# Kernel optimization log

Measured on AMD Instinct MI355X. Metric: run time of the kernel, lower is better.

## Reference

```python
import jax, jax.numpy as jnp
import numpy as np

# Dimensions (see shape_source)
B, N, F = 2, 400, 246          # batch, nodes, node features
S = 1                           # edge feature channels
C = 32                          # stack_channels
LBL = 1440                      # shape_node_labels
STACK_IN = 2 * F + 2 * S        # concat([x_i, x_j, e_ij, e_ji])
NODE_IN = F + 2 * C             # concat([x, agg_in, agg_out])


def _glorot(key, shape):
    fan_in, fan_out = shape[0], shape[1]
    lim = np.sqrt(6.0 / (fan_in + fan_out)).astype(np.float32)
    return jax.random.uniform(key, shape, jnp.float32, -lim, lim)


def setup_inputs() -> dict:
    key = jax.random.key(0)
    ks = jax.random.split(key, 12)
    x = jax.random.normal(ks[0], (B, N, F), jnp.float32)
    a = (jax.random.uniform(ks[1], (B, N, N)) < 0.10).astype(jnp.float32)
    e = jax.random.uniform(ks[2], (B, N, N, S), jnp.float32)
    return {
        "x": x,
        "a": a,
        "e": e,
        # XENetConv stack model: single Dense(C) + PReLU (per-channel alpha)
        "W_stack": _glorot(ks[3], (STACK_IN, C)),
        "b_stack": jnp.zeros((C,), jnp.float32),
        "alpha": jnp.full((C,), 0.25, jnp.float32),
        # attention heads: Dense(1, sigmoid) each
        "W_att_i": _glorot(ks[4], (C, 1)),
        "b_att_i": jnp.zeros((1,), jnp.float32),
        "W_att_j": _glorot(ks[5], (C, 1)),
        "b_att_j": jnp.zeros((1,), jnp.float32),
        # node model: Dense(F) over concat([x, agg_in, agg_out]) (linear)
        "W_node": _glorot(ks[6], (NODE_IN, F)),
        "b_node": jnp.zeros((F,), jnp.float32),
        # trailing Dense(shape_node_labels, linear)
        "W_out": _glorot(ks[7], (F, LBL)),
        "b_out": jnp.zeros((LBL,), jnp.float32),
    }


def reference(x, a, e, W_stack, b_stack, alpha, W_att_i, b_att_i,
              W_att_j, b_att_j, W_node, b_node, W_out, b_out):
    # --- XENetConvBatch ---
    # pairwise stack: [x_i, x_j, e_ij, e_ji] over all (i, j) node pairs
    x_i = jnp.broadcast_to(x[:, :, None, :], (B, N, N, F))
    x_j = jnp.broadcast_to(x[:, None, :, :], (B, N, N, F))
    e_t = jnp.transpose(e, (0, 2, 1, 3))                     # e_ji
    stack = jnp.concatenate([x_i, x_j, e, e_t], axis=-1)     # (B,N,N,2F+2S)
    s = jnp.einsum("bijk,kc->bijc", stack, W_stack) + b_stack  # (B,N,N,C)
    s = jnp.where(s >= 0, s, alpha * s)                      # PReLU
    s = s * a[..., None]                                     # mask non-edges
    # attention (sigmoid gates for incoming / outgoing aggregation)
    att_i = jax.nn.sigmoid(s @ W_att_i + b_att_i)            # (B,N,N,1)
    att_j = jax.nn.sigmoid(s @ W_att_j + b_att_j)
    agg_i = jnp.sum(s * att_i, axis=2)                       # (B,N,C) sum over j
    agg_j = jnp.sum(s * att_j, axis=1)                       # (B,N,C) sum over i
    x_new = jnp.concatenate([x, agg_i, agg_j], axis=-1) @ W_node + b_node  # (B,N,F)
    # Net discards the edge output of the conv; final linear Dense
    out = x_new @ W_out + b_out                              # (B,N,LBL)
    return out
```

## Files before the change

### kernel.cpp

```cpp
#include <hip/hip_runtime.h>
#include <math.h>

#define B_ 2
#define N_ 400
#define F_ 246
#define C_ 32
#define LBL_ 1440

#define KX_ 320
#define KN_ 256

typedef __attribute__((ext_vector_type(8))) short bf16x8;
typedef __attribute__((ext_vector_type(4))) float f32x4;

__device__ __forceinline__ short f2bf(float f) {
    unsigned u = __float_as_uint(f);
    return (short)((u + 0x7FFF + ((u >> 16) & 1)) >> 16);
}

#define T_ABUF (800 * KX_)
#define T_W2T  (64 * KX_)
#define T_WNT  (256 * KX_)
#define T_WOT  (LBL_ * KN_)
__global__ void k_prep(const float* __restrict__ x, const float* __restrict__ Ws,
                       const float* __restrict__ Wn, const float* __restrict__ Wo,
                       short* __restrict__ Abuf, short* __restrict__ W2T,
                       short* __restrict__ WnT, short* __restrict__ WoT) {
    int t = blockIdx.x * 256 + threadIdx.x;
    if (t < T_ABUF) {
        int row = t / KX_, k = t % KX_;
        Abuf[t] = (k < F_) ? f2bf(x[row * F_ + k]) : (short)0;
        return;
    }
    t -= T_ABUF;
    if (t < T_W2T) {
        int n = t / KX_, k = t % KX_;
        float v = 0.f;
        if (k < F_) v = (n < C_) ? Ws[k * C_ + n] : Ws[(F_ + k) * C_ + (n - C_)];
        W2T[t] = f2bf(v);
        return;
    }
    t -= T_W2T;
    if (t < T_WNT) {
        int n = t / KX_, k = t % KX_;
        float v = (n < F_ && k < F_ + 2 * C_) ? Wn[k * F_ + n] : 0.f;
        WnT[t] = f2bf(v);
        return;
    }
    t -= T_WNT;
    if (t < T_WOT) {
        int n = t / KN_, k = t % KN_;
        WoT[t] = (k < F_) ? f2bf(Wo[k * LBL_ + n]) : (short)0;
    }
}

template <int K>
__device__ __forceinline__ f32x4 mfma_tile(const short* __restrict__ A,
                                           const short* __restrict__ BT,
                                           int m0, int n0, int lane) {
    int r = lane & 15, quad = lane >> 4;
    const short* ap = A + (size_t)(m0 + r) * K + quad * 8;
    const short* bp = BT + (size_t)(n0 + r) * K + quad * 8;
    f32x4 acc = {0.f, 0.f, 0.f, 0.f};
    #pragma unroll
    for (int kk = 0; kk < K; kk += 32) {
        bf16x8 a = *(const bf16x8*)(ap + kk);
        bf16x8 b = *(const bf16x8*)(bp + kk);
        acc = __builtin_amdgcn_mfma_f32_16x16x32_bf16(a, b, acc, 0, 0, 0);
    }
    return acc;
}

__global__ void k_pq(const short* __restrict__ Abuf, const short* __restrict__ W2T,
                     float* __restrict__ PQ) {
    int lane = threadIdx.x;
    int m0 = blockIdx.x * 16, n0 = blockIdx.y * 16;
    f32x4 acc = mfma_tile<KX_>(Abuf, W2T, m0, n0, lane);
    int n = n0 + (lane & 15), mb = m0 + (lane >> 4) * 4;
    #pragma unroll
    for (int reg = 0; reg < 4; ++reg)
        PQ[(size_t)(mb + reg) * 64 + n] = acc[reg];
}

__global__ void k_agg(const float* __restrict__ a, const float* __restrict__ e,
                      const float* __restrict__ Ws, const float* __restrict__ bs,
                      const float* __restrict__ alpha,
                      const float* __restrict__ Wai, const float* __restrict__ bai,
                      const float* __restrict__ Waj, const float* __restrict__ baj,
                      const float* __restrict__ PQ,
                      float* __restrict__ AGGI, float* __restrict__ AGGJ) {
    int blk  = blockIdx.x;
    int mode = (blk >= B_ * N_) ? 1 : 0;
    int row  = mode ? blk - B_ * N_ : blk;
    int b = row / N_, n = row % N_;
    int tid = threadIdx.x;
    int c = tid & 31, g = tid >> 5;

    float w3  = Ws[(2 * F_) * C_ + c];
    float w4  = Ws[(2 * F_ + 1) * C_ + c];
    float bsc = bs[c];
    float alc = alpha[c];
    float wat = mode ? Waj[c] : Wai[c];
    float bat = mode ? baj[0] : bai[0];

    float ownc = PQ[(size_t)row * 64 + (mode ? 32 : 0) + c];
    const float* oth = PQ + (size_t)b * N_ * 64 + (mode ? 0 : 32) + c;

    const float* abase = a + (size_t)b * N_ * N_;
    const float* ebase = e + (size_t)b * N_ * N_;

    float acc = 0.f;
    #pragma unroll 4
    for (int m = g; m < N_; m += 8) {
        float aij  = mode ? abase[m * N_ + n] : abase[n * N_ + m];
        float er   = ebase[n * N_ + m];
        float ec   = ebase[m * N_ + n];
        float othv = oth[(size_t)m * 64];
        if (aij != 0.f) {
            float eij = mode ? ec : er;
            float eji = mode ? er : ec;
            float raw = ownc + othv + eij * w3 + eji * w4 + bsc;
            float s = (raw >= 0.f ? raw : alc * raw) * aij;
            float t = s * wat;
            t += __shfl_xor(t, 1, 32);
            t += __shfl_xor(t, 2, 32);
            t += __shfl_xor(t, 4, 32);
            t += __shfl_xor(t, 8, 32);
            t += __shfl_xor(t, 16, 32);
            float att = 1.f / (1.f + __expf(-(t + bat)));
            acc += s * att;
        }
    }
    __shared__ float part[8][C_ + 1];
    part[g][c] = acc;
    __syncthreads();
    if (tid < C_) {
        float tot = 0.f;
        #pragma unroll
        for (int gg = 0; gg < 8; ++gg) tot += part[gg][tid];
        (mode ? AGGJ : AGGI)[row * C_ + tid] = tot;
    }
}

__global__ void k_fill(const float* __restrict__ AGGI, const float* __restrict__ AGGJ,
                       short* __restrict__ Abuf) {
    int t = blockIdx.x * 256 + threadIdx.x;
    int row = t >> 6, c = t & 63;
    float v = (c < C_) ? AGGI[row * C_ + c] : AGGJ[row * C_ + (c - C_)];
    Abuf[(size_t)row * KX_ + F_ + c] = f2bf(v);
}

__global__ void k_node(const short* __restrict__ Abuf, const short* __restrict__ WnT,
                       const float* __restrict__ bn, short* __restrict__ XN16) {
    int lane = threadIdx.x;
    int m0 = blockIdx.x * 16, n0 = blockIdx.y * 16;
    f32x4 acc = mfma_tile<KX_>(Abuf, WnT, m0, n0, lane);
    int n = n0 + (lane & 15), mb = m0 + (lane >> 4) * 4;
    float bv = (n < F_) ? bn[n] : 0.f;
    #pragma unroll
    for (int reg = 0; reg < 4; ++reg)
        XN16[(size_t)(mb + reg) * KN_ + n] = (n < F_) ? f2bf(acc[reg] + bv) : (short)0;
}

__global__ void k_out(const short* __restrict__ XN16, const short* __restrict__ WoT,
                      const float* __restrict__ bo, float* __restrict__ out) {
    int lane = threadIdx.x;
    int m0 = blockIdx.x * 16, n0 = blockIdx.y * 16;
    f32x4 acc = mfma_tile<KN_>(XN16, WoT, m0, n0, lane);
    int n = n0 + (lane & 15), mb = m0 + (lane >> 4) * 4;
    float bv = bo[n];
    #pragma unroll
    for (int reg = 0; reg < 4; ++reg)
        out[(size_t)(mb + reg) * LBL_ + n] = acc[reg] + bv;
}

extern "C" void kernel_launch(void* const* d_in, const int* in_sizes, int n_in,
                              void* d_out, int out_size, void* d_ws, size_t ws_size,
                              hipStream_t stream) {
    const float* x   = (const float*)d_in[0];
    const float* a   = (const float*)d_in[1];
    const float* e   = (const float*)d_in[2];
    const float* Ws  = (const float*)d_in[3];
    const float* bs  = (const float*)d_in[4];
    const float* al  = (const float*)d_in[5];
    const float* Wai = (const float*)d_in[6];
    const float* bai = (const float*)d_in[7];
    const float* Waj = (const float*)d_in[8];
    const float* baj = (const float*)d_in[9];
    const float* Wn  = (const float*)d_in[10];
    const float* bn  = (const float*)d_in[11];
    const float* Wo  = (const float*)d_in[12];
    const float* bo  = (const float*)d_in[13];

    float* PQ   = (float*)d_ws;
    float* AGGI = PQ + 800 * 64;
    float* AGGJ = AGGI + 800 * C_;
    short* Abuf = (short*)(AGGJ + 800 * C_);
    short* W2T  = Abuf + T_ABUF;
    short* WnT  = W2T + T_W2T;
    short* WoT  = WnT + T_WNT;
    short* XN16 = WoT + T_WOT;

    int prep_total = T_ABUF + T_W2T + T_WNT + T_WOT;
    k_prep<<<(prep_total + 255) / 256, 256, 0, stream>>>(x, Ws, Wn, Wo,
                                                         Abuf, W2T, WnT, WoT);
    k_pq  <<<dim3(50, 4),  64, 0, stream>>>(Abuf, W2T, PQ);
    k_agg <<<2 * B_ * N_, 256, 0, stream>>>(a, e, Ws, bs, al, Wai, bai, Waj, baj,
                                            PQ, AGGI, AGGJ);
    k_fill<<<(800 * 64) / 256, 256, 0, stream>>>(AGGI, AGGJ, Abuf);
    k_node<<<dim3(50, 16), 64, 0, stream>>>(Abuf, WnT, bn, XN16);
    k_out <<<dim3(50, 90), 64, 0, stream>>>(XN16, WoT, bo, (float*)d_out);
}
```

Measured before the change: 132.2 us.

## Fuse all stages into one persistent kernel with grid-wide barriers

Replaces the six separate launches (prep, PQ GEMM, aggregation, fill, node GEMM, output GEMM) with one persistent kernel of 512 blocks that runs every stage in grid-stride loops, separated by atomic-counter grid barriers. The aggregation stage now writes bf16 results straight into the GEMM input buffer, which removes the fill pass and the fp32 AGG buffers. The weight-transpose loops are reindexed so the fp32 source reads are coalesced. This trades per-launch overhead and inter-kernel gaps for barrier spin cost, and it depends on all 512 blocks being co-resident, since the barrier can deadlock otherwise.

Measured after the change: 528.7 us. 4x slower.

```diff
diff --git a/kernel.cpp b/kernel.cpp
--- a/kernel.cpp
+++ b/kernel.cpp
@@ -10,48 +10,47 @@
 #define KX_ 320
 #define KN_ 256
 
-typedef __attribute__((ext_vector_type(8))) short bf16x8;
-typedef __attribute__((ext_vector_type(4))) float f32x4;
-
-__device__ __forceinline__ short f2bf(float f) {
-    unsigned u = __float_as_uint(f);
-    return (short)((u + 0x7FFF + ((u >> 16) & 1)) >> 16);
-}
+#define GRID_ 512
+#define TPB_  256
 
 #define T_ABUF (800 * KX_)
 #define T_W2T  (64 * KX_)
 #define T_WNT  (256 * KX_)
 #define T_WOT  (LBL_ * KN_)
-__global__ void k_prep(const float* __restrict__ x, const float* __restrict__ Ws,
-                       const float* __restrict__ Wn, const float* __restrict__ Wo,
-                       short* __restrict__ Abuf, short* __restrict__ W2T,
-                       short* __restrict__ WnT, short* __restrict__ WoT) {
-    int t = blockIdx.x * 256 + threadIdx.x;
-    if (t < T_ABUF) {
-        int row = t / KX_, k = t % KX_;
-        Abuf[t] = (k < F_) ? f2bf(x[row * F_ + k]) : (short)0;
-        return;
-    }
-    t -= T_ABUF;
-    if (t < T_W2T) {
-        int n = t / KX_, k = t % KX_;
-        float v = 0.f;
-        if (k < F_) v = (n < C_) ? Ws[k * C_ + n] : Ws[(F_ + k) * C_ + (n - C_)];
-        W2T[t] = f2bf(v);
-        return;
-    }
-    t -= T_W2T;
-    if (t < T_WNT) {
-        int n = t / KX_, k = t % KX_;
-        float v = (n < F_ && k < F_ + 2 * C_) ? Wn[k * F_ + n] : 0.f;
-        WnT[t] = f2bf(v);
-        return;
-    }
-    t -= T_WNT;
-    if (t < T_WOT) {
-        int n = t / KN_, k = t % KN_;
-        WoT[t] = (k < F_) ? f2bf(Wo[k * LBL_ + n]) : (short)0;
-    }
+
+typedef __attribute__((ext_vector_type(8))) short bf16x8;
+typedef __attribute__((ext_vector_type(4))) float f32x4;
+
+__device__ __forceinline__ short f2bf(float f) {
+    unsigned u = __float_as_uint(f);
+    return (short)((u + 0x7FFF + ((u >> 16) & 1)) >> 16);
+}
+
+struct KP {
+    const float *x, *a, *e, *Ws, *bs, *al, *Wai, *bai, *Waj, *baj, *Wn, *bn, *Wo, *bo;
+    float *out, *PQ;
+    short *Abuf, *W2T, *WnT, *WoT, *XN16;
+    int *bar;
+};
+
+__device__ __forceinline__ void gbar(int* cnt, int* gen, int it) {
+    __syncthreads();
+    if (threadIdx.x == 0) {
+        if (__hip_atomic_fetch_add(cnt, 1, __ATOMIC_ACQ_REL,
+                                   __HIP_MEMORY_SCOPE_AGENT) == GRID_ - 1) {
+            __hip_atomic_store(cnt, 0, __ATOMIC_RELAXED, __HIP_MEMORY_SCOPE_AGENT);
+            __hip_atomic_store(gen, it + 1, __ATOMIC_RELEASE, __HIP_MEMORY_SCOPE_AGENT);
+        } else {
+            while (__hip_atomic_load(gen, __ATOMIC_ACQUIRE,
+                                     __HIP_MEMORY_SCOPE_AGENT) <= it)
+                __builtin_amdgcn_s_sleep(2);
+        }
+    }
+    __syncthreads();
+}
+
+__global__ void k_zero(int* bar) {
+    if (threadIdx.x < 2) bar[threadIdx.x] = 0;
 }
 
 template <int K>
@@ -64,150 +63,160 @@
     f32x4 acc = {0.f, 0.f, 0.f, 0.f};
     #pragma unroll
     for (int kk = 0; kk < K; kk += 32) {
-        bf16x8 a = *(const bf16x8*)(ap + kk);
-        bf16x8 b = *(const bf16x8*)(bp + kk);
-        acc = __builtin_amdgcn_mfma_f32_16x16x32_bf16(a, b, acc, 0, 0, 0);
+        bf16x8 av = *(const bf16x8*)(ap + kk);
+        bf16x8 bv = *(const bf16x8*)(bp + kk);
+        acc = __builtin_amdgcn_mfma_f32_16x16x32_bf16(av, bv, acc, 0, 0, 0);
     }
     return acc;
 }
 
-__global__ void k_pq(const short* __restrict__ Abuf, const short* __restrict__ W2T,
-                     float* __restrict__ PQ) {
-    int lane = threadIdx.x;
-    int m0 = blockIdx.x * 16, n0 = blockIdx.y * 16;
-    f32x4 acc = mfma_tile<KX_>(Abuf, W2T, m0, n0, lane);
-    int n = n0 + (lane & 15), mb = m0 + (lane >> 4) * 4;
-    #pragma unroll
-    for (int reg = 0; reg < 4; ++reg)
-        PQ[(size_t)(mb + reg) * 64 + n] = acc[reg];
-}
-
-__global__ void k_agg(const float* __restrict__ a, const float* __restrict__ e,
-                      const float* __restrict__ Ws, const float* __restrict__ bs,
-                      const float* __restrict__ alpha,
-                      const float* __restrict__ Wai, const float* __restrict__ bai,
-                      const float* __restrict__ Waj, const float* __restrict__ baj,
-                      const float* __restrict__ PQ,
-                      float* __restrict__ AGGI, float* __restrict__ AGGJ) {
-    int blk  = blockIdx.x;
-    int mode = (blk >= B_ * N_) ? 1 : 0;
-    int row  = mode ? blk - B_ * N_ : blk;
-    int b = row / N_, n = row % N_;
-    int tid = threadIdx.x;
-    int c = tid & 31, g = tid >> 5;
-
-    float w3  = Ws[(2 * F_) * C_ + c];
-    float w4  = Ws[(2 * F_ + 1) * C_ + c];
-    float bsc = bs[c];
-    float alc = alpha[c];
-    float wat = mode ? Waj[c] : Wai[c];
-    float bat = mode ? baj[0] : bai[0];
-
-    float ownc = PQ[(size_t)row * 64 + (mode ? 32 : 0) + c];
-    const float* oth = PQ + (size_t)b * N_ * 64 + (mode ? 0 : 32) + c;
-
-    const float* abase = a + (size_t)b * N_ * N_;
-    const float* ebase = e + (size_t)b * N_ * N_;
-
-    float acc = 0.f;
-    #pragma unroll 4
-    for (int m = g; m < N_; m += 8) {
-        float aij  = mode ? abase[m * N_ + n] : abase[n * N_ + m];
-        float er   = ebase[n * N_ + m];
-        float ec   = ebase[m * N_ + n];
-        float othv = oth[(size_t)m * 64];
-        if (aij != 0.f) {
-            float eij = mode ? ec : er;
-            float eji = mode ? er : ec;
-            float raw = ownc + othv + eij * w3 + eji * w4 + bsc;
-            float s = (raw >= 0.f ? raw : alc * raw) * aij;
-            float t = s * wat;
-            t += __shfl_xor(t, 1, 32);
-            t += __shfl_xor(t, 2, 32);
-            t += __shfl_xor(t, 4, 32);
-            t += __shfl_xor(t, 8, 32);
-            t += __shfl_xor(t, 16, 32);
-            float att = 1.f / (1.f + __expf(-(t + bat)));
-            acc += s * att;
+__global__ __launch_bounds__(TPB_, 2) void k_fused(KP p) {
+    int tid  = threadIdx.x;
+    int gt   = blockIdx.x * TPB_ + tid;
+    int wv   = gt >> 6;
+    int lane = tid & 63;
+    const int NT = GRID_ * TPB_;
+    const int NW = NT / 64;
+    int* cnt = p.bar;
+    int* gen = p.bar + 1;
+
+    for (int t = gt; t < T_ABUF; t += NT) {
+        int row = t / KX_, k = t % KX_;
+        p.Abuf[t] = (k < F_) ? f2bf(p.x[row * F_ + k]) : (short)0;
+    }
+    for (int t = gt; t < T_W2T; t += NT) {
+        int n = t & 63, k = t >> 6;
+        float v = 0.f;
+        if (k < F_) v = (n < C_) ? p.Ws[k * C_ + n] : p.Ws[(F_ + k) * C_ + (n - C_)];
+        p.W2T[(size_t)n * KX_ + k] = f2bf(v);
+    }
+    for (int t = gt; t < T_WNT; t += NT) {
+        int n = t & 255, k = t >> 8;
+        float v = (n < F_ && k < F_ + 2 * C_) ? p.Wn[k * F_ + n] : 0.f;
+        p.WnT[(size_t)n * KX_ + k] = f2bf(v);
+    }
+    for (int t = gt; t < T_WOT; t += NT) {
+        int n = t % LBL_, k = t / LBL_;
+        p.WoT[(size_t)n * KN_ + k] = (k < F_) ? f2bf(p.Wo[k * LBL_ + n]) : (short)0;
+    }
+    gbar(cnt, gen, 0);
+
+    for (int t = wv; t < 50 * 4; t += NW) {
+        int m0 = (t % 50) * 16, n0 = (t / 50) * 16;
+        f32x4 acc = mfma_tile<KX_>(p.Abuf, p.W2T, m0, n0, lane);
+        int n = n0 + (lane & 15), mb = m0 + (lane >> 4) * 4;
+        #pragma unroll
+        for (int r = 0; r < 4; ++r)
+            p.PQ[(size_t)(mb + r) * 64 + n] = acc[r];
+    }
+    gbar(cnt, gen, 1);
+
+    {
+        __shared__ float part[8][C_ + 1];
+        int c = tid & 31, g = tid >> 5;
+        for (int v = blockIdx.x; v < 2 * B_ * N_; v += GRID_) {
+            int mode = (v >= B_ * N_) ? 1 : 0;
+            int row  = mode ? v - B_ * N_ : v;
+            int b = row / N_, n = row % N_;
+
+            float w3  = p.Ws[(2 * F_) * C_ + c];
+            float w4  = p.Ws[(2 * F_ + 1) * C_ + c];
+            float bsc = p.bs[c];
+            float alc = p.al[c];
+            float wat = mode ? p.Waj[c] : p.Wai[c];
+            float bat = mode ? p.baj[0] : p.bai[0];
+
+            float ownc = p.PQ[(size_t)row * 64 + (mode ? 32 : 0) + c];
+            const float* oth = p.PQ + (size_t)b * N_ * 64 + (mode ? 0 : 32) + c;
+            const float* abase = p.a + (size_t)b * N_ * N_;
+            const float* ebase = p.e + (size_t)b * N_ * N_;
+
+            float acc = 0.f;
+            #pragma unroll 4
+            for (int m = g; m < N_; m += 8) {
+                float aij  = mode ? abase[m * N_ + n] : abase[n * N_ + m];
+                float er   = ebase[n * N_ + m];
+                float ec   = ebase[m * N_ + n];
+                float othv = oth[(size_t)m * 64];
+                if (aij != 0.f) {
+                    float eij = mode ? ec : er;
+                    float eji = mode ? er : ec;
+                    float raw = ownc + othv + eij * w3 + eji * w4 + bsc;
+                    float s = (raw >= 0.f ? raw : alc * raw) * aij;
+                    float t2 = s * wat;
+                    t2 += __shfl_xor(t2, 1, 32);
+                    t2 += __shfl_xor(t2, 2, 32);
+                    t2 += __shfl_xor(t2, 4, 32);
+                    t2 += __shfl_xor(t2, 8, 32);
+                    t2 += __shfl_xor(t2, 16, 32);
+                    float att = 1.f / (1.f + __expf(-(t2 + bat)));
+                    acc += s * att;
+                }
+            }
+            part[g][c] = acc;
+            __syncthreads();
+            if (tid < C_) {
+                float tot = 0.f;
+                #pragma unroll
+                for (int gg = 0; gg < 8; ++gg) tot += part[gg][tid];
+                p.Abuf[(size_t)row * KX_ + F_ + mode * C_ + tid] = f2bf(tot);
+            }
+            __syncthreads();
         }
     }
-    __shared__ float part[8][C_ + 1];
-    part[g][c] = acc;
-    __syncthreads();
-    if (tid < C_) {
-        float tot = 0.f;
+    gbar(cnt, gen, 2);
+
+    for (int t = wv; t < 50 * 16; t += NW) {
+        int m0 = (t % 50) * 16, n0 = (t / 50) * 16;
+        f32x4 acc = mfma_tile<KX_>(p.Abuf, p.WnT, m0, n0, lane);
+        int n = n0 + (lane & 15), mb = m0 + (lane >> 4) * 4;
+        float bv = (n < F_) ? p.bn[n] : 0.f;
         #pragma unroll
-        for (int gg = 0; gg < 8; ++gg) tot += part[gg][tid];
-        (mode ? AGGJ : AGGI)[row * C_ + tid] = tot;
-    }
-}
-
-__global__ void k_fill(const float* __restrict__ AGGI, const float* __restrict__ AGGJ,
-                       short* __restrict__ Abuf) {
-    int t = blockIdx.x * 256 + threadIdx.x;
-    int row = t >> 6, c = t & 63;
-    float v = (c < C_) ? AGGI[row * C_ + c] : AGGJ[row * C_ + (c - C_)];
-    Abuf[(size_t)row * KX_ + F_ + c] = f2bf(v);
-}
-
-__global__ void k_node(const short* __restrict__ Abuf, const short* __restrict__ WnT,
-                       const float* __restrict__ bn, short* __restrict__ XN16) {
-    int lane = threadIdx.x;
-    int m0 = blockIdx.x * 16, n0 = blockIdx.y * 16;
-    f32x4 acc = mfma_tile<KX_>(Abuf, WnT, m0, n0, lane);
-    int n = n0 + (lane & 15), mb = m0 + (lane >> 4) * 4;
-    float bv = (n < F_) ? bn[n] : 0.f;
-    #pragma unroll
-    for (int reg = 0; reg < 4; ++reg)
-        XN16[(size_t)(mb + reg) * KN_ + n] = (n < F_) ? f2bf(acc[reg] + bv) : (short)0;
-}
-
-__global__ void k_out(const short* __restrict__ XN16, const short* __restrict__ WoT,
-                      const float* __restrict__ bo, float* __restrict__ out) {
-    int lane = threadIdx.x;
-    int m0 = blockIdx.x * 16, n0 = blockIdx.y * 16;
-    f32x4 acc = mfma_tile<KN_>(XN16, WoT, m0, n0, lane);
-    int n = n0 + (lane & 15), mb = m0 + (lane >> 4) * 4;
-    float bv = bo[n];
-    #pragma unroll
-    for (int reg = 0; reg < 4; ++reg)
-        out[(size_t)(mb + reg) * LBL_ + n] = acc[reg] + bv;
+        for (int r = 0; r < 4; ++r)
+            p.XN16[(size_t)(mb + r) * KN_ + n] =
+                (n < F_) ? f2bf(acc[r] + bv) : (short)0;
+    }
+    gbar(cnt, gen, 3);
+
+    for (int t = wv; t < 50 * 90; t += NW) {
+        int m0 = (t % 50) * 16, n0 = (t / 50) * 16;
+        f32x4 acc = mfma_tile<KN_>(p.XN16, p.WoT, m0, n0, lane);
+        int n = n0 + (lane & 15), mb = m0 + (lane >> 4) * 4;
+        float bv = p.bo[n];
+        #pragma unroll
+        for (int r = 0; r < 4; ++r)
+            p.out[(size_t)(mb + r) * LBL_ + n] = acc[r] + bv;
+    }
 }
 
 extern "C" void kernel_launch(void* const* d_in, const int* in_sizes, int n_in,
                               void* d_out, int out_size, void* d_ws, size_t ws_size,
                               hipStream_t stream) {
-    const float* x   = (const float*)d_in[0];
-    const float* a   = (const float*)d_in[1];
-    const float* e   = (const float*)d_in[2];
-    const float* Ws  = (const float*)d_in[3];
-    const float* bs  = (const float*)d_in[4];
-    const float* al  = (const float*)d_in[5];
-    const float* Wai = (const float*)d_in[6];
-    const float* bai = (const float*)d_in[7];
-    const float* Waj = (const float*)d_in[8];
-    const float* baj = (const float*)d_in[9];
-    const float* Wn  = (const float*)d_in[10];
-    const float* bn  = (const float*)d_in[11];
-    const float* Wo  = (const float*)d_in[12];
-    const float* bo  = (const float*)d_in[13];
-
-    float* PQ   = (float*)d_ws;
-    float* AGGI = PQ + 800 * 64;
-    float* AGGJ = AGGI + 800 * C_;
-    short* Abuf = (short*)(AGGJ + 800 * C_);
-    short* W2T  = Abuf + T_ABUF;
-    short* WnT  = W2T + T_W2T;
-    short* WoT  = WnT + T_WNT;
-    short* XN16 = WoT + T_WOT;
-
-    int prep_total = T_ABUF + T_W2T + T_WNT + T_WOT;
-    k_prep<<<(prep_total + 255) / 256, 256, 0, stream>>>(x, Ws, Wn, Wo,
-                                                         Abuf, W2T, WnT, WoT);
-    k_pq  <<<dim3(50, 4),  64, 0, stream>>>(Abuf, W2T, PQ);
-    k_agg <<<2 * B_ * N_, 256, 0, stream>>>(a, e, Ws, bs, al, Wai, bai, Waj, baj,
-                                            PQ, AGGI, AGGJ);
-    k_fill<<<(800 * 64) / 256, 256, 0, stream>>>(AGGI, AGGJ, Abuf);
-    k_node<<<dim3(50, 16), 64, 0, stream>>>(Abuf, WnT, bn, XN16);
-    k_out <<<dim3(50, 90), 64, 0, stream>>>(XN16, WoT, bo, (float*)d_out);
-}
+    KP p;
+    p.x   = (const float*)d_in[0];
+    p.a   = (const float*)d_in[1];
+    p.e   = (const float*)d_in[2];
+    p.Ws  = (const float*)d_in[3];
+    p.bs  = (const float*)d_in[4];
+    p.al  = (const float*)d_in[5];
+    p.Wai = (const float*)d_in[6];
+    p.bai = (const float*)d_in[7];
+    p.Waj = (const float*)d_in[8];
+    p.baj = (const float*)d_in[9];
+    p.Wn  = (const float*)d_in[10];
+    p.bn  = (const float*)d_in[11];
+    p.Wo  = (const float*)d_in[12];
+    p.bo  = (const float*)d_in[13];
+    p.out = (float*)d_out;
+
+    p.bar  = (int*)d_ws;
+    p.PQ   = (float*)d_ws + 4;
+    p.Abuf = (short*)(p.PQ + 800 * 64);
+    p.W2T  = p.Abuf + T_ABUF;
+    p.WnT  = p.W2T + T_W2T;
+    p.WoT  = p.WnT + T_WNT;
+    p.XN16 = p.WoT + T_WOT;
+
+    k_zero <<<1, 64, 0, stream>>>(p.bar);
+    k_fused<<<GRID_, TPB_, 0, stream>>>(p);
+}
```

## Fuse aggregate fill into k_agg, tile weight transposes, widen GEMM tiles

Applied to the files above, without the earlier changes.

The k_fill kernel is removed: k_agg now writes its bf16 aggregates straight into the padded activation buffer, which saves a launch and an intermediate buffer. k_prep is restructured so that each x row is handled by one block, and the Wo and Wn transposes go through a 32x32 shared-memory tile to get coalesced reads and writes. The node and output GEMM kernels now compute two 16-column tiles per wave so the A fragments are reused, which halves their grid sizes. Zero padding of Abuf columns 310..319 is no longer written by k_prep, so correctness relies on the matching WnT columns being zero.

After: 126.7 us, median of 2. -4.2%, faster.

```diff
diff --git a/kernel.cpp b/kernel.cpp
--- a/kernel.cpp
+++ b/kernel.cpp
@@ -6,51 +6,73 @@
 #define F_ 246
 #define C_ 32
 #define LBL_ 1440
+#define NODE_IN_ 310
 
 #define KX_ 320
 #define KN_ 256
-
-typedef __attribute__((ext_vector_type(8))) short bf16x8;
-typedef __attribute__((ext_vector_type(4))) float f32x4;
-
-__device__ __forceinline__ short f2bf(float f) {
-    unsigned u = __float_as_uint(f);
-    return (short)((u + 0x7FFF + ((u >> 16) & 1)) >> 16);
-}
 
 #define T_ABUF (800 * KX_)
 #define T_W2T  (64 * KX_)
 #define T_WNT  (256 * KX_)
 #define T_WOT  (LBL_ * KN_)
+
+typedef __attribute__((ext_vector_type(8))) short bf16x8;
+typedef __attribute__((ext_vector_type(4))) float f32x4;
+
+__device__ __forceinline__ short f2bf(float f) {
+    unsigned u = __float_as_uint(f);
+    return (short)((u + 0x7FFF + ((u >> 16) & 1)) >> 16);
+}
+
 __global__ void k_prep(const float* __restrict__ x, const float* __restrict__ Ws,
                        const float* __restrict__ Wn, const float* __restrict__ Wo,
                        short* __restrict__ Abuf, short* __restrict__ W2T,
                        short* __restrict__ WnT, short* __restrict__ WoT) {
-    int t = blockIdx.x * 256 + threadIdx.x;
-    if (t < T_ABUF) {
-        int row = t / KX_, k = t % KX_;
-        Abuf[t] = (k < F_) ? f2bf(x[row * F_ + k]) : (short)0;
+    __shared__ short tile[32][33];
+    int bx = blockIdx.x, tid = threadIdx.x;
+    if (bx < 800) {
+        if (tid < F_) Abuf[bx * KX_ + tid] = f2bf(x[bx * F_ + tid]);
         return;
     }
-    t -= T_ABUF;
-    if (t < T_W2T) {
-        int n = t / KX_, k = t % KX_;
-        float v = 0.f;
-        if (k < F_) v = (n < C_) ? Ws[k * C_ + n] : Ws[(F_ + k) * C_ + (n - C_)];
-        W2T[t] = f2bf(v);
+    bx -= 800;
+    int tx = tid & 31, ty = tid >> 5;
+    if (bx < 360) {
+        int n0 = (bx % 45) * 32, k0 = (bx / 45) * 32;
+        #pragma unroll
+        for (int r = 0; r < 4; ++r) {
+            int k = k0 + ty + r * 8;
+            tile[ty + r * 8][tx] = (k < F_) ? f2bf(Wo[k * LBL_ + n0 + tx]) : (short)0;
+        }
+        __syncthreads();
+        #pragma unroll
+        for (int r = 0; r < 4; ++r)
+            WoT[(size_t)(n0 + ty + r * 8) * KN_ + k0 + tx] = tile[tx][ty + r * 8];
         return;
     }
-    t -= T_W2T;
-    if (t < T_WNT) {
-        int n = t / KX_, k = t % KX_;
-        float v = (n < F_ && k < F_ + 2 * C_) ? Wn[k * F_ + n] : 0.f;
-        WnT[t] = f2bf(v);
+    bx -= 360;
+    if (bx < 80) {
+        int n0 = (bx % 8) * 32, k0 = (bx / 8) * 32;
+        #pragma unroll
+        for (int r = 0; r < 4; ++r) {
+            int k = k0 + ty + r * 8, n = n0 + tx;
+            tile[ty + r * 8][tx] =
+                (n < F_ && k < NODE_IN_) ? f2bf(Wn[k * F_ + n]) : (short)0;
+        }
+        __syncthreads();
+        #pragma unroll
+        for (int r = 0; r < 4; ++r)
+            WnT[(size_t)(n0 + ty + r * 8) * KX_ + k0 + tx] = tile[tx][ty + r * 8];
         return;
     }
-    t -= T_WNT;
-    if (t < T_WOT) {
-        int n = t / KN_, k = t % KN_;
-        WoT[t] = (k < F_) ? f2bf(Wo[k * LBL_ + n]) : (short)0;
+    bx -= 80;
+    {
+        int t = bx * 256 + tid;
+        if (t < 64 * KX_) {
+            int n = t / KX_, k = t - n * KX_;
+            float v = 0.f;
+            if (k < F_) v = (n < C_) ? Ws[k * C_ + n] : Ws[(F_ + k) * C_ + (n - C_)];
+            W2T[t] = f2bf(v);
+        }
     }
 }
 
@@ -64,11 +86,30 @@
     f32x4 acc = {0.f, 0.f, 0.f, 0.f};
     #pragma unroll
     for (int kk = 0; kk < K; kk += 32) {
-        bf16x8 a = *(const bf16x8*)(ap + kk);
-        bf16x8 b = *(const bf16x8*)(bp + kk);
-        acc = __builtin_amdgcn_mfma_f32_16x16x32_bf16(a, b, acc, 0, 0, 0);
+        bf16x8 av = *(const bf16x8*)(ap + kk);
+        bf16x8 bv = *(const bf16x8*)(bp + kk);
+        acc = __builtin_amdgcn_mfma_f32_16x16x32_bf16(av, bv, acc, 0, 0, 0);
     }
     return acc;
+}
+
+template <int K>
+__device__ __forceinline__ void mfma_tile2(const short* __restrict__ A,
+                                           const short* __restrict__ BT,
+                                           int m0, int n0, int lane,
+                                           f32x4& acc0, f32x4& acc1) {
+    int r = lane & 15, quad = lane >> 4;
+    const short* ap = A + (size_t)(m0 + r) * K + quad * 8;
+    const short* b0 = BT + (size_t)(n0 + r) * K + quad * 8;
+    const short* b1 = BT + (size_t)(n0 + 16 + r) * K + quad * 8;
+    #pragma unroll
+    for (int kk = 0; kk < K; kk += 32) {
+        bf16x8 av  = *(const bf16x8*)(ap + kk);
+        bf16x8 bv0 = *(const bf16x8*)(b0 + kk);
+        bf16x8 bv1 = *(const bf16x8*)(b1 + kk);
+        acc0 = __builtin_amdgcn_mfma_f32_16x16x32_bf16(av, bv0, acc0, 0, 0, 0);
+        acc1 = __builtin_amdgcn_mfma_f32_16x16x32_bf16(av, bv1, acc1, 0, 0, 0);
+    }
 }
 
 __global__ void k_pq(const short* __restrict__ Abuf, const short* __restrict__ W2T,
@@ -78,8 +119,8 @@
     f32x4 acc = mfma_tile<KX_>(Abuf, W2T, m0, n0, lane);
     int n = n0 + (lane & 15), mb = m0 + (lane >> 4) * 4;
     #pragma unroll
-    for (int reg = 0; reg < 4; ++reg)
-        PQ[(size_t)(mb + reg) * 64 + n] = acc[reg];
+    for (int r = 0; r < 4; ++r)
+        PQ[(size_t)(mb + r) * 64 + n] = acc[r];
 }
 
 __global__ void k_agg(const float* __restrict__ a, const float* __restrict__ e,
@@ -87,8 +128,7 @@
                       const float* __restrict__ alpha,
                       const float* __restrict__ Wai, const float* __restrict__ bai,
                       const float* __restrict__ Waj, const float* __restrict__ baj,
-                      const float* __restrict__ PQ,
-                      float* __restrict__ AGGI, float* __restrict__ AGGJ) {
+                      const float* __restrict__ PQ, short* __restrict__ Abuf) {
     int blk  = blockIdx.x;
     int mode = (blk >= B_ * N_) ? 1 : 0;
     int row  = mode ? blk - B_ * N_ : blk;
@@ -105,7 +145,6 @@
 
     float ownc = PQ[(size_t)row * 64 + (mode ? 32 : 0) + c];
     const float* oth = PQ + (size_t)b * N_ * 64 + (mode ? 0 : 32) + c;
-
     const float* abase = a + (size_t)b * N_ * N_;
     const float* ebase = e + (size_t)b * N_ * N_;
 
@@ -121,13 +160,13 @@
             float eji = mode ? er : ec;
             float raw = ownc + othv + eij * w3 + eji * w4 + bsc;
             float s = (raw >= 0.f ? raw : alc * raw) * aij;
-            float t = s * wat;
-            t += __shfl_xor(t, 1, 32);
-            t += __shfl_xor(t, 2, 32);
-            t += __shfl_xor(t, 4, 32);
-            t += __shfl_xor(t, 8, 32);
-            t += __shfl_xor(t, 16, 32);
-            float att = 1.f / (1.f + __expf(-(t + bat)));
+            float t2 = s * wat;
+            t2 += __shfl_xor(t2, 1, 32);
+            t2 += __shfl_xor(t2, 2, 32);
+            t2 += __shfl_xor(t2, 4, 32);
+            t2 += __shfl_xor(t2, 8, 32);
+            t2 += __shfl_xor(t2, 16, 32);
+            float att = 1.f / (1.f + __expf(-(t2 + bat)));
             acc += s * att;
         }
     }
@@ -138,40 +177,45 @@
         float tot = 0.f;
         #pragma unroll
         for (int gg = 0; gg < 8; ++gg) tot += part[gg][tid];
-        (mode ? AGGJ : AGGI)[row * C_ + tid] = tot;
-    }
-}
-
-__global__ void k_fill(const float* __restrict__ AGGI, const float* __restrict__ AGGJ,
-                       short* __restrict__ Abuf) {
-    int t = blockIdx.x * 256 + threadIdx.x;
-    int row = t >> 6, c = t & 63;
-    float v = (c < C_) ? AGGI[row * C_ + c] : AGGJ[row * C_ + (c - C_)];
-    Abuf[(size_t)row * KX_ + F_ + c] = f2bf(v);
+        Abuf[(size_t)row * KX_ + F_ + mode * C_ + tid] = f2bf(tot);
+    }
 }
 
 __global__ void k_node(const short* __restrict__ Abuf, const short* __restrict__ WnT,
                        const float* __restrict__ bn, short* __restrict__ XN16) {
     int lane = threadIdx.x;
-    int m0 = blockIdx.x * 16, n0 = blockIdx.y * 16;
-    f32x4 acc = mfma_tile<KX_>(Abuf, WnT, m0, n0, lane);
-    int n = n0 + (lane & 15), mb = m0 + (lane >> 4) * 4;
-    float bv = (n < F_) ? bn[n] : 0.f;
-    #pragma unroll
-    for (int reg = 0; reg < 4; ++reg)
-        XN16[(size_t)(mb + reg) * KN_ + n] = (n < F_) ? f2bf(acc[reg] + bv) : (short)0;
+    int m0 = blockIdx.x * 16, n0 = blockIdx.y * 32;
+    f32x4 a0 = {0,0,0,0}, a1 = {0,0,0,0};
+    mfma_tile2<KX_>(Abuf, WnT, m0, n0, lane, a0, a1);
+    int col = lane & 15, mb = m0 + (lane >> 4) * 4;
+    #pragma unroll
+    for (int h = 0; h < 2; ++h) {
+        int nn = n0 + h * 16 + col;
+        f32x4 acc = h ? a1 : a0;
+        float bv = (nn < F_) ? bn[nn] : 0.f;
+        #pragma unroll
+        for (int r = 0; r < 4; ++r)
+            XN16[(size_t)(mb + r) * KN_ + nn] =
+                (nn < F_) ? f2bf(acc[r] + bv) : (short)0;
+    }
 }
 
 __global__ void k_out(const short* __restrict__ XN16, const short* __restrict__ WoT,
                       const float* __restrict__ bo, float* __restrict__ out) {
     int lane = threadIdx.x;
-    int m0 = blockIdx.x * 16, n0 = blockIdx.y * 16;
-    f32x4 acc = mfma_tile<KN_>(XN16, WoT, m0, n0, lane);
-    int n = n0 + (lane & 15), mb = m0 + (lane >> 4) * 4;
-    float bv = bo[n];
-    #pragma unroll
-    for (int reg = 0; reg < 4; ++reg)
-        out[(size_t)(mb + reg) * LBL_ + n] = acc[reg] + bv;
+    int m0 = blockIdx.x * 16, n0 = blockIdx.y * 32;
+    f32x4 a0 = {0,0,0,0}, a1 = {0,0,0,0};
+    mfma_tile2<KN_>(XN16, WoT, m0, n0, lane, a0, a1);
+    int col = lane & 15, mb = m0 + (lane >> 4) * 4;
+    #pragma unroll
+    for (int h = 0; h < 2; ++h) {
+        int nn = n0 + h * 16 + col;
+        f32x4 acc = h ? a1 : a0;
+        float bv = bo[nn];
+        #pragma unroll
+        for (int r = 0; r < 4; ++r)
+            out[(size_t)(mb + r) * LBL_ + nn] = acc[r] + bv;
+    }
 }
 
 extern "C" void kernel_launch(void* const* d_in, const int* in_sizes, int n_in,
@@ -193,21 +237,16 @@
     const float* bo  = (const float*)d_in[13];
 
     float* PQ   = (float*)d_ws;
-    float* AGGI = PQ + 800 * 64;
-    float* AGGJ = AGGI + 800 * C_;
-    short* Abuf = (short*)(AGGJ + 800 * C_);
+    short* Abuf = (short*)(PQ + 800 * 64);
     short* W2T  = Abuf + T_ABUF;
     short* WnT  = W2T + T_W2T;
     short* WoT  = WnT + T_WNT;
     short* XN16 = WoT + T_WOT;
 
-    int prep_total = T_ABUF + T_W2T + T_WNT + T_WOT;
-    k_prep<<<(prep_total + 255) / 256, 256, 0, stream>>>(x, Ws, Wn, Wo,
-                                                         Abuf, W2T, WnT, WoT);
+    k_prep<<<1320, 256, 0, stream>>>(x, Ws, Wn, Wo, Abuf, W2T, WnT, WoT);
     k_pq  <<<dim3(50, 4),  64, 0, stream>>>(Abuf, W2T, PQ);
     k_agg <<<2 * B_ * N_, 256, 0, stream>>>(a, e, Ws, bs, al, Wai, bai, Waj, baj,
-                                            PQ, AGGI, AGGJ);
-    k_fill<<<(800 * 64) / 256, 256, 0, stream>>>(AGGI, AGGJ, Abuf);
-    k_node<<<dim3(50, 16), 64, 0, stream>>>(Abuf, WnT, bn, XN16);
-    k_out <<<dim3(50, 90), 64, 0, stream>>>(XN16, WoT, bo, (float*)d_out);
-}
+                                            PQ, Abuf);
+    k_node<<<dim3(50, 8),  64, 0, stream>>>(Abuf, WnT, bn, XN16);
+    k_out <<<dim3(50, 45), 64, 0, stream>>>(XN16, WoT, bo, (float*)d_out);
+}
```
